# Kernel optimization log

Measured on AMD Instinct MI355X. Metric: run time of the kernel, lower is better.

## Reference

```python
import jax, jax.numpy as jnp
import numpy as np

N = 50000
E = 800000
NODE_IN = 64
EDGE_IN = 8
OUT = 1
SAGE_DIMS = [(64, 64), (64, 64), (64, 32), (32, 32)]
EDGE_DIMS = [(8, 64), (64, 64), (64, 32), (32, 32)]


def setup_inputs():
    key = jax.random.key(0)
    keys = iter(jax.random.split(key, 64))
    d = {}
    d["x"] = jax.random.normal(next(keys), (N, NODE_IN), jnp.float32)
    d["dis"] = jax.random.normal(next(keys), (E, EDGE_IN), jnp.float32)
    d["edge_index"] = jax.random.randint(next(keys), (2, E), 0, N, dtype=jnp.int32)
    for i, (fi, fo) in enumerate(SAGE_DIMS):
        d[f"s{i}_wl"] = jax.random.normal(next(keys), (fi, fo), jnp.float32) / np.sqrt(fi).astype(np.float32)
        d[f"s{i}_bl"] = jnp.zeros((fo,), jnp.float32)
        d[f"s{i}_wr"] = jax.random.normal(next(keys), (fi, fo), jnp.float32) / np.sqrt(fi).astype(np.float32)
    for i, (fi, h) in enumerate(EDGE_DIMS):
        d[f"e{i}_w1"] = jax.random.normal(next(keys), (fi, 2 * h), jnp.float32) / np.sqrt(fi).astype(np.float32)
        d[f"e{i}_b1"] = jnp.zeros((2 * h,), jnp.float32)
        d[f"e{i}_w2"] = jax.random.normal(next(keys), (2 * h, h), jnp.float32) / np.sqrt(2 * h).astype(np.float32)
        d[f"e{i}_b2"] = jnp.zeros((h,), jnp.float32)
    d["fc_w"] = jax.random.normal(next(keys), (64, OUT), jnp.float32) / 8.0
    d["fc_b"] = jnp.zeros((OUT,), jnp.float32)
    return d


def _sage(x, row, col, wl, bl, wr):
    # PyG SAGEConv (aggr='mean'): lin_l(mean_{j->i} x_j) + lin_r(x_i); lin_l has bias.
    msg = x[row]  # [E, F] gather of source features
    s = jax.ops.segment_sum(msg, col, num_segments=N)
    cnt = jax.ops.segment_sum(jnp.ones((row.shape[0], 1), x.dtype), col, num_segments=N)
    mean = s / jnp.maximum(cnt, 1.0)  # isolated nodes -> 0 (matches scatter-mean)
    return mean @ wl + bl + x @ wr


def _edge_conv(dis, col, w1, b1, w2, b2):
    # EdgeOnlyConv: add_self_loops with num_nodes=E and zero edge_attr, so the
    # output has E rows; self-loop message = lin(0) = b1 and each segment t gets
    # mean = (sum_{edges->t} lin(dis) + b1) / (deg_in(t) + 1); then lin_update.
    msg = dis @ w1 + b1  # [E, 2h]
    s = jax.ops.segment_sum(msg, col, num_segments=E)
    deg = jax.ops.segment_sum(jnp.ones((col.shape[0], 1), dis.dtype), col, num_segments=E)
    aggr = (s + b1) / (deg + 1.0)
    return aggr @ w2 + b2


def _forward(x, dis, edge_index, sage_params, edge_params, fc_w, fc_b):
    row, col = edge_index[0], edge_index[1]
    h = x
    for wl, bl, wr in sage_params:
        h = jax.nn.leaky_relu(_sage(h, row, col, wl, bl, wr))
    d = dis
    for w1, b1, w2, b2 in edge_params:
        d = jax.nn.leaky_relu(_edge_conv(d, col, w1, b1, w2, b2))
    # dropout is identity at inference
    feats = jnp.concatenate([h[row] * h[col], d], axis=1)  # [E, hidden]
    return feats @ fc_w + fc_b


def reference(x, dis, edge_index, s0_wl, s0_bl, s0_wr, s1_wl, s1_bl, s1_wr, s2_wl, s2_bl, s2_wr, s3_wl, s3_bl, s3_wr, e0_w1, e0_b1, e0_w2, e0_b2, e1_w1, e1_b1, e1_w2, e1_b2, e2_w1, e2_b1, e2_w2, e2_b2, e3_w1, e3_b1, e3_w2, e3_b2, fc_w, fc_b):
    sage_params = [(s0_wl, s0_bl, s0_wr), (s1_wl, s1_bl, s1_wr), (s2_wl, s2_bl, s2_wr), (s3_wl, s3_bl, s3_wr)]
    edge_params = [(e0_w1, e0_b1, e0_w2, e0_b2), (e1_w1, e1_b1, e1_w2, e1_b2), (e2_w1, e2_b1, e2_w2, e2_b2), (e3_w1, e3_b1, e3_w2, e3_b2)]
    return _forward(x, dis, edge_index, sage_params, edge_params, fc_w, fc_b)
```

## Files before the change

### kernel.cpp

```cpp
#include <hip/hip_runtime.h>

#define LRELU(v) ((v) > 0.0f ? (v) : 0.01f * (v))

__global__ void bucket_count_k(const int* __restrict__ col, int* __restrict__ bcnt, int E) {
    __shared__ int lcnt[512];
    int tid = threadIdx.x;
    for (int i = tid; i < 512; i += 1024) lcnt[i] = 0;
    __syncthreads();
    int base = blockIdx.x * 8192;
    for (int k = 0; k < 8; ++k) {
        int e = base + k * 1024 + tid;
        if (e < E) atomicAdd(&lcnt[col[e] >> 7], 1);
    }
    __syncthreads();
    for (int i = tid; i < 512; i += 1024) {
        int v = lcnt[i];
        if (v) atomicAdd(&bcnt[i], v);
    }
}

__global__ void bucket_scan_k(const int* __restrict__ bcnt, int* __restrict__ bbase,
                              int* __restrict__ bwp, int NBUCK, int E) {
    __shared__ int s[512];
    int tid = threadIdx.x;
    int v = (tid < NBUCK) ? bcnt[tid] : 0;
    s[tid] = v;
    __syncthreads();
    for (int off = 1; off < 512; off <<= 1) {
        int t = (tid >= off) ? s[tid - off] : 0;
        __syncthreads();
        s[tid] += t;
        __syncthreads();
    }
    if (tid < NBUCK) {
        int ex = s[tid] - v;
        bbase[tid] = ex;
        bwp[tid] = ex;
    }
    if (tid == 0) bbase[NBUCK] = E;
}

__global__ void bucket_scatter_k(const int* __restrict__ row, const int* __restrict__ col,
                                 int* __restrict__ bwp, int2* __restrict__ tmp, int E) {
    __shared__ int lcnt[512];
    __shared__ int gbase[512];
    int tid = threadIdx.x;
    for (int i = tid; i < 512; i += 1024) lcnt[i] = 0;
    __syncthreads();
    int base = blockIdx.x * 8192;
    int lpos[8], bk[8];
    for (int k = 0; k < 8; ++k) {
        int e = base + k * 1024 + tid;
        if (e < E) {
            int b = col[e] >> 7;
            bk[k] = b;
            lpos[k] = atomicAdd(&lcnt[b], 1);
        } else
            bk[k] = -1;
    }
    __syncthreads();
    for (int i = tid; i < 512; i += 1024) {
        int v = lcnt[i];
        gbase[i] = v ? atomicAdd(&bwp[i], v) : 0;
    }
    __syncthreads();
    for (int k = 0; k < 8; ++k) {
        int e = base + k * 1024 + tid;
        if (e < E) {
            int c = col[e];
            tmp[gbase[bk[k]] + lpos[k]] = make_int2(row[e], ((c & 127) << 25) | e);
        }
    }
}

__global__ void bucket_csr_k(const int2* __restrict__ tmp, const int* __restrict__ bbase,
                             int* __restrict__ rowptr, int* __restrict__ cnt,
                             int2* __restrict__ pairs, int N, int E) {
    constexpr int CAP = 6144;
    __shared__ int2 buf[CAP];
    __shared__ int lcnt[128];
    __shared__ int sscan[128];
    __shared__ int lwp[128];
    int b = blockIdx.x;
    int tid = threadIdx.x;
    int s = bbase[b], e = bbase[b + 1];
    int sz = e - s;
    if (tid < 128) lcnt[tid] = 0;
    __syncthreads();
    for (int i = tid; i < sz; i += 256) {
        int2 v = tmp[s + i];
        if (i < CAP) buf[i] = v;
        atomicAdd(&lcnt[((unsigned)v.y) >> 25], 1);
    }
    __syncthreads();
    if (tid < 128) sscan[tid] = lcnt[tid];
    __syncthreads();
    for (int off = 1; off < 128; off <<= 1) {
        int t = (tid < 128 && tid >= off) ? sscan[tid - off] : 0;
        __syncthreads();
        if (tid < 128) sscan[tid] += t;
        __syncthreads();
    }
    if (tid < 128) {
        int ex = sscan[tid] - lcnt[tid];
        lwp[tid] = ex;
        int c = b * 128 + tid;
        if (c < N) {
            rowptr[c] = s + ex;
            cnt[c] = lcnt[tid];
            if (c == N - 1) rowptr[N] = E;
        }
    }
    __syncthreads();
    for (int i = tid; i < sz; i += 256) {
        int2 v = (i < CAP) ? buf[i] : tmp[s + i];
        int cl = ((unsigned)v.y) >> 25;
        int p = atomicAdd(&lwp[cl], 1);
        pairs[s + p] = make_int2(v.x, v.y & 0x1FFFFFF);
    }
}

template <int FIN, int FOUT>
__global__ void gemm2_k(const float* __restrict__ h, const float* __restrict__ wl,
                        const float* __restrict__ wr, const float* __restrict__ bl,
                        float* __restrict__ hl, float* __restrict__ hr, int N) {
    constexpr int XT = (2 * FOUT) / 4;
    constexpr int YT = 256 / XT;
    constexpr int NPT = 4;
    constexpr int NPB = YT * NPT;
    __shared__ float sw[FIN * 2 * FOUT];
    int lin = threadIdx.y * XT + threadIdx.x;
    for (int idx = lin; idx < FIN * FOUT; idx += 256) {
        int f = idx / FOUT, o = idx % FOUT;
        sw[f * 2 * FOUT + o] = wl[idx];
        sw[f * 2 * FOUT + FOUT + o] = wr[idx];
    }
    __syncthreads();
    int og = threadIdx.x * 4;
    int base = blockIdx.x * NPB + threadIdx.y * NPT;
    int ix[NPT] = {min(base + 0, N - 1), min(base + 1, N - 1), min(base + 2, N - 1),
                   min(base + 3, N - 1)};
    float4 s[NPT] = {{0.f, 0.f, 0.f, 0.f}, {0.f, 0.f, 0.f, 0.f}, {0.f, 0.f, 0.f, 0.f},
                     {0.f, 0.f, 0.f, 0.f}};
#pragma unroll 2
    for (int f = 0; f < FIN; f += 4) {
        float4 w0 = *(const float4*)&sw[(f + 0) * 2 * FOUT + og];
        float4 w1 = *(const float4*)&sw[(f + 1) * 2 * FOUT + og];
        float4 w2 = *(const float4*)&sw[(f + 2) * 2 * FOUT + og];
        float4 w3 = *(const float4*)&sw[(f + 3) * 2 * FOUT + og];
#pragma unroll
        for (int k = 0; k < NPT; ++k) {
            float4 v = *(const float4*)(h + (size_t)ix[k] * FIN + f);
            s[k].x += v.x * w0.x + v.y * w1.x + v.z * w2.x + v.w * w3.x;
            s[k].y += v.x * w0.y + v.y * w1.y + v.z * w2.y + v.w * w3.y;
            s[k].z += v.x * w0.z + v.y * w1.z + v.z * w2.z + v.w * w3.z;
            s[k].w += v.x * w0.w + v.y * w1.w + v.z * w2.w + v.w * w3.w;
        }
    }
    bool isR = og >= FOUT;
    int oo = isR ? og - FOUT : og;
    float4 bias = {0.f, 0.f, 0.f, 0.f};
    if (isR) bias = *(const float4*)&bl[oo];
    float* dst = isR ? hr : hl;
#pragma unroll
    for (int k = 0; k < NPT; ++k) {
        int i = base + k;
        if (i < N) {
            float4 r = {s[k].x + bias.x, s[k].y + bias.y, s[k].z + bias.z, s[k].w + bias.w};
            *(float4*)(dst + (size_t)i * FOUT + oo) = r;
        }
    }
}

__global__ void aggr_fused64_k(const float* __restrict__ hl, const float* __restrict__ hr,
                               const int* __restrict__ rowptr, const int2* __restrict__ pairs,
                               float* __restrict__ out, int N) {
    int wave = (blockIdx.x * blockDim.x + threadIdx.x) >> 6;
    int lane = threadIdx.x & 63;
    if (wave >= N) return;
    int u = lane >> 4, f4 = lane & 15;
    int s = rowptr[wave], e = rowptr[wave + 1];
    float4 a = {0.f, 0.f, 0.f, 0.f};
    for (int p = s + u; p < e; p += 4) {
        const float4* hp = (const float4*)(hl + (size_t)pairs[p].x * 64);
        float4 v = hp[f4];
        a.x += v.x; a.y += v.y; a.z += v.z; a.w += v.w;
    }
    a.x += __shfl_down(a.x, 32); a.y += __shfl_down(a.y, 32);
    a.z += __shfl_down(a.z, 32); a.w += __shfl_down(a.w, 32);
    a.x += __shfl_down(a.x, 16); a.y += __shfl_down(a.y, 16);
    a.z += __shfl_down(a.z, 16); a.w += __shfl_down(a.w, 16);
    if (lane < 16) {
        float inv = 1.0f / fmaxf((float)(e - s), 1.0f);
        float4 r = ((const float4*)(hr + (size_t)wave * 64))[f4];
        float4 o;
        o.x = LRELU(a.x * inv + r.x);
        o.y = LRELU(a.y * inv + r.y);
        o.z = LRELU(a.z * inv + r.z);
        o.w = LRELU(a.w * inv + r.w);
        ((float4*)(out + (size_t)wave * 64))[f4] = o;
    }
}

__global__ void aggr_fused32_k(const float* __restrict__ hl, const float* __restrict__ hr,
                               const int* __restrict__ rowptr, const int2* __restrict__ pairs,
                               float* __restrict__ out, int N) {
    int wave = (blockIdx.x * blockDim.x + threadIdx.x) >> 6;
    int lane = threadIdx.x & 63;
    if (wave >= N) return;
    int u = lane >> 3, f4 = lane & 7;
    int s = rowptr[wave], e = rowptr[wave + 1];
    float4 a = {0.f, 0.f, 0.f, 0.f};
    for (int p = s + u; p < e; p += 8) {
        const float4* hp = (const float4*)(hl + (size_t)pairs[p].x * 32);
        float4 v = hp[f4];
        a.x += v.x; a.y += v.y; a.z += v.z; a.w += v.w;
    }
    a.x += __shfl_down(a.x, 32); a.y += __shfl_down(a.y, 32);
    a.z += __shfl_down(a.z, 32); a.w += __shfl_down(a.w, 32);
    a.x += __shfl_down(a.x, 16); a.y += __shfl_down(a.y, 16);
    a.z += __shfl_down(a.z, 16); a.w += __shfl_down(a.w, 16);
    a.x += __shfl_down(a.x, 8); a.y += __shfl_down(a.y, 8);
    a.z += __shfl_down(a.z, 8); a.w += __shfl_down(a.w, 8);
    if (lane < 8) {
        float inv = 1.0f / fmaxf((float)(e - s), 1.0f);
        float4 r = ((const float4*)(hr + (size_t)wave * 32))[f4];
        float4 o;
        o.x = LRELU(a.x * inv + r.x);
        o.y = LRELU(a.y * inv + r.y);
        o.z = LRELU(a.z * inv + r.z);
        o.w = LRELU(a.w * inv + r.w);
        ((float4*)(out + (size_t)wave * 32))[f4] = o;
    }
}

__global__ void edge_aggr8_k(const float* __restrict__ dis, const int* __restrict__ rowptr,
                             const int2* __restrict__ pairs, float* __restrict__ sd, int N) {
    int wave = (blockIdx.x * blockDim.x + threadIdx.x) >> 6;
    int lane = threadIdx.x & 63;
    if (wave >= N) return;
    int u = lane >> 1, f4 = lane & 1;
    int s = rowptr[wave], e = rowptr[wave + 1];
    float4 a = {0.f, 0.f, 0.f, 0.f};
    for (int p = s + u; p < e; p += 32) {
        const float4* dp = (const float4*)(dis + (size_t)pairs[p].y * 8);
        float4 v = dp[f4];
        a.x += v.x; a.y += v.y; a.z += v.z; a.w += v.w;
    }
    for (int off = 32; off >= 2; off >>= 1) {
        a.x += __shfl_down(a.x, off); a.y += __shfl_down(a.y, off);
        a.z += __shfl_down(a.z, off); a.w += __shfl_down(a.w, off);
    }
    if (lane < 2) ((float4*)(sd + (size_t)wave * 8))[f4] = a;
}

template <int H2, int HOUT>
__device__ __forceinline__ void w12_body(const float* __restrict__ w1,
                                         const float* __restrict__ w2, float* __restrict__ out,
                                         int i, int o) {
    float s = 0.0f;
#pragma unroll
    for (int k = 0; k < H2; ++k) s += w1[i * H2 + k] * w2[k * HOUT + o];
    out[i * HOUT + o] = s;
}

__global__ void gemm_w12_all_k(const float* __restrict__ w1_0, const float* __restrict__ w2_0,
                               float* __restrict__ o0, const float* __restrict__ w1_1,
                               const float* __restrict__ w2_1, float* __restrict__ o1,
                               const float* __restrict__ w1_2, const float* __restrict__ w2_2,
                               float* __restrict__ o2, const float* __restrict__ w1_3,
                               const float* __restrict__ w2_3, float* __restrict__ o3) {
    int b = blockIdx.x;
    int o = threadIdx.x;
    if (b < 8) {
        w12_body<128, 64>(w1_0, w2_0, o0, b, o);
    } else if (b < 72) {
        w12_body<128, 64>(w1_1, w2_1, o1, b - 8, o);
    } else if (b < 136) {
        if (o < 32) w12_body<64, 32>(w1_2, w2_2, o2, b - 72, o);
    } else {
        if (o < 32) w12_body<64, 32>(w1_3, w2_3, o3, b - 136, o);
    }
}

template <int FIN, int FOUT>
__global__ void edge_compute_scatter_k(const float* __restrict__ sd, const int* __restrict__ cnt,
                                       const float* __restrict__ w12, const float* __restrict__ mw2,
                                       const float* __restrict__ b1w2, const float* __restrict__ b2,
                                       const float* __restrict__ cnext,
                                       const int* __restrict__ col, float* __restrict__ sdnext,
                                       int N) {
    constexpr int ROWS = 256 / FOUT;
    constexpr int NPT = 4;
    constexpr int NPB = ROWS * NPT;
    __shared__ float sw[FIN * FOUT];
    int lin = threadIdx.y * FOUT + threadIdx.x;
    for (int idx = lin; idx < FIN * FOUT; idx += 256) sw[idx] = w12[idx];
    __syncthreads();
    int o = threadIdx.x;
    int base = blockIdx.x * NPB + threadIdx.y * NPT;
    int ix[NPT] = {min(base + 0, N - 1), min(base + 1, N - 1), min(base + 2, N - 1),
                   min(base + 3, N - 1)};
    float s[NPT] = {0.f, 0.f, 0.f, 0.f};
#pragma unroll 2
    for (int f = 0; f < FIN; f += 4) {
        float w0 = sw[(f + 0) * FOUT + o], w1 = sw[(f + 1) * FOUT + o];
        float w2 = sw[(f + 2) * FOUT + o], w3 = sw[(f + 3) * FOUT + o];
#pragma unroll
        for (int k = 0; k < NPT; ++k) {
            float4 v = *(const float4*)(sd + (size_t)ix[k] * FIN + f);
            s[k] += v.x * w0 + v.y * w1 + v.z * w2 + v.w * w3;
        }
    }
    float mo = mw2[o], bo = b1w2[o], b2o = b2[o], co = cnext[o];
#pragma unroll
    for (int k = 0; k < NPT; ++k) {
        int i = base + k;
        if (i < N) {
            float deg = (float)cnt[i];
            float inv = 1.0f / (deg + 1.0f);
            float val = LRELU((s[k] + deg * mo + bo) * inv + b2o);
            atomicAdd(&sdnext[(size_t)col[i] * FOUT + o], val - co);
        }
    }
}

template <int FIN, int FOUT>
__global__ void edge_compute2_k(const float* __restrict__ sd, const int* __restrict__ cnt,
                                const float* __restrict__ w12, const float* __restrict__ mw2,
                                const float* __restrict__ b1w2, const float* __restrict__ b2,
                                float* __restrict__ out, int N) {
    constexpr int ROWS = 256 / FOUT;
    constexpr int NPT = 4;
    constexpr int NPB = ROWS * NPT;
    __shared__ float sw[FIN * FOUT];
    int lin = threadIdx.y * FOUT + threadIdx.x;
    for (int idx = lin; idx < FIN * FOUT; idx += 256) sw[idx] = w12[idx];
    __syncthreads();
    int o = threadIdx.x;
    int base = blockIdx.x * NPB + threadIdx.y * NPT;
    int ix[NPT] = {min(base + 0, N - 1), min(base + 1, N - 1), min(base + 2, N - 1),
                   min(base + 3, N - 1)};
    float s[NPT] = {0.f, 0.f, 0.f, 0.f};
#pragma unroll 2
    for (int f = 0; f < FIN; f += 4) {
        float w0 = sw[(f + 0) * FOUT + o], w1 = sw[(f + 1) * FOUT + o];
        float w2 = sw[(f + 2) * FOUT + o], w3 = sw[(f + 3) * FOUT + o];
#pragma unroll
        for (int k = 0; k < NPT; ++k) {
            float4 v = *(const float4*)(sd + (size_t)ix[k] * FIN + f);
            s[k] += v.x * w0 + v.y * w1 + v.z * w2 + v.w * w3;
        }
    }
    float mo = mw2[o], bo = b1w2[o], b2o = b2[o];
#pragma unroll
    for (int k = 0; k < NPT; ++k) {
        int i = base + k;
        if (i < N) {
            float deg = (float)cnt[i];
            float inv = 1.0f / (deg + 1.0f);
            out[(size_t)i * FOUT + o] = LRELU((s[k] + deg * mo + bo) * inv + b2o);
        }
    }
}

__global__ void consts_k(const float* __restrict__ e0_b1, const float* __restrict__ e0_w2,
                         const float* __restrict__ e0_b2, const float* __restrict__ e1_b1,
                         const float* __restrict__ e1_w2, const float* __restrict__ e1_b2,
                         const float* __restrict__ e2_b1, const float* __restrict__ e2_w2,
                         const float* __restrict__ e2_b2, const float* __restrict__ e3_b1,
                         const float* __restrict__ e3_w2, const float* __restrict__ e3_b2,
                         const float* __restrict__ w12_1, const float* __restrict__ w12_2,
                         const float* __restrict__ w12_3, float* __restrict__ cbuf) {
    __shared__ float c1[64], c2[64], c3[32];
    int tid = threadIdx.x;
    if (tid < 64) {
        float s = 0.0f;
#pragma unroll
        for (int k = 0; k < 128; ++k) s += e0_b1[k] * e0_w2[k * 64 + tid];
        cbuf[192 + tid] = s;
        c1[tid] = LRELU(s + e0_b2[tid]);
        cbuf[tid] = c1[tid];
    }
    if (tid < 64) {
        float s = 0.0f;
#pragma unroll
        for (int k = 0; k < 128; ++k) s += e1_b1[k] * e1_w2[k * 64 + tid];
        cbuf[256 + tid] = s;
        c2[tid] = LRELU(s + e1_b2[tid]);
        cbuf[64 + tid] = c2[tid];
    }
    if (tid < 32) {
        float s = 0.0f;
#pragma unroll
        for (int k = 0; k < 64; ++k) s += e2_b1[k] * e2_w2[k * 32 + tid];
        cbuf[384 + tid] = s;
        c3[tid] = LRELU(s + e2_b2[tid]);
        cbuf[128 + tid] = c3[tid];
    }
    if (tid < 32) {
        float s = 0.0f;
#pragma unroll
        for (int k = 0; k < 64; ++k) s += e3_b1[k] * e3_w2[k * 32 + tid];
        cbuf[448 + tid] = s;
        cbuf[160 + tid] = LRELU(s + e3_b2[tid]);
    }
    __syncthreads();
    if (tid < 64) {
        float s = cbuf[256 + tid];
#pragma unroll
        for (int f = 0; f < 64; ++f) s += c1[f] * w12_1[f * 64 + tid];
        cbuf[320 + tid] = s;
    }
    if (tid < 32) {
        float s = cbuf[384 + tid];
#pragma unroll
        for (int f = 0; f < 64; ++f) s += c2[f] * w12_2[f * 32 + tid];
        cbuf[416 + tid] = s;
    }
    if (tid < 32) {
        float s = cbuf[448 + tid];
#pragma unroll
        for (int f = 0; f < 32; ++f) s += c3[f] * w12_3[f * 32 + tid];
        cbuf[480 + tid] = s;
    }
}

__global__ void tobf16_k(const float* __restrict__ src, unsigned short* __restrict__ dst, int n) {
    int base = (blockIdx.x * 256 + threadIdx.x) * 4;
    if (base >= n) return;
    float4 v = *(const float4*)(src + base);
    union { float f; unsigned u; } c;
    unsigned short o[4];
    c.f = v.x; o[0] = (unsigned short)((c.u + 0x7fffu + ((c.u >> 16) & 1)) >> 16);
    c.f = v.y; o[1] = (unsigned short)((c.u + 0x7fffu + ((c.u >> 16) & 1)) >> 16);
    c.f = v.z; o[2] = (unsigned short)((c.u + 0x7fffu + ((c.u >> 16) & 1)) >> 16);
    c.f = v.w; o[3] = (unsigned short)((c.u + 0x7fffu + ((c.u >> 16) & 1)) >> 16);
    *(ushort4*)(dst + base) = make_ushort4(o[0], o[1], o[2], o[3]);
}

__device__ __forceinline__ float b2f_lo(unsigned u) {
    union { unsigned i; float f; } v;
    v.i = u << 16;
    return v.f;
}
__device__ __forceinline__ float b2f_hi(unsigned u) {
    union { unsigned i; float f; } v;
    v.i = u & 0xffff0000u;
    return v.f;
}
__device__ __forceinline__ float bdot8(uint4 a, uint4 b, const float* __restrict__ w) {
    return b2f_lo(a.x) * b2f_lo(b.x) * w[0] + b2f_hi(a.x) * b2f_hi(b.x) * w[1] +
           b2f_lo(a.y) * b2f_lo(b.y) * w[2] + b2f_hi(a.y) * b2f_hi(b.y) * w[3] +
           b2f_lo(a.z) * b2f_lo(b.z) * w[4] + b2f_hi(a.z) * b2f_hi(b.z) * w[5] +
           b2f_lo(a.w) * b2f_lo(b.w) * w[6] + b2f_hi(a.w) * b2f_hi(b.w) * w[7];
}

__global__ void final_k(const unsigned short* __restrict__ h3b, const float* __restrict__ dv3,
                        const float* __restrict__ c4, const int* __restrict__ row,
                        const int* __restrict__ col, const float* __restrict__ fcw,
                        const float* __restrict__ fcb, float* __restrict__ out, int E, int N) {
    __shared__ float sw[64];
    __shared__ float sc4[32];
    __shared__ float cdot_s;
    int tid = threadIdx.x;
    if (tid < 64) sw[tid] = fcw[tid];
    if (tid < 32) sc4[tid] = c4[tid];
    __syncthreads();
    if (tid == 0) {
        float cd = 0.0f;
#pragma unroll
        for (int k = 0; k < 32; ++k) cd += sc4[k] * sw[32 + k];
        cdot_s = cd;
    }
    __syncthreads();
    float fb = fcb[0];
    float cdot = cdot_s;
    int e0 = blockIdx.x * 512 + tid;
    int e1 = e0 + 256;
    bool v0 = e0 < E, v1 = e1 < E;
    int r0 = 0, c0 = 0, r1 = 0, c1 = 0;
    if (v0) { r0 = row[e0]; c0 = col[e0]; }
    if (v1) { r1 = row[e1]; c1 = col[e1]; }
    uint4 a00, a01, b00, b01, a10, a11, b10, b11;
    if (v0) {
        const uint4* pr = (const uint4*)(h3b + (size_t)r0 * 32);
        const uint4* pc = (const uint4*)(h3b + (size_t)c0 * 32);
        a00 = pr[0]; a01 = pr[1]; b00 = pc[0]; b01 = pc[1];
    }
    if (v1) {
        const uint4* pr = (const uint4*)(h3b + (size_t)r1 * 32);
        const uint4* pc = (const uint4*)(h3b + (size_t)c1 * 32);
        a10 = pr[0]; a11 = pr[1]; b10 = pc[0]; b11 = pc[1];
    }
    if (v0) {
        float s = fb + bdot8(a00, b00, sw) + bdot8(a01, b01, sw + 8) ;
        const uint4* pr = (const uint4*)(h3b + (size_t)r0 * 32);
        const uint4* pc = (const uint4*)(h3b + (size_t)c0 * 32);
        uint4 a2 = pr[2], a3 = pr[3], b2 = pc[2], b3 = pc[3];
        s += bdot8(a2, b2, sw + 16) + bdot8(a3, b3, sw + 24);
        if (e0 < N) {
            const float4* dp = (const float4*)(dv3 + (size_t)e0 * 32);
#pragma unroll
            for (int q = 0; q < 8; ++q) {
                float4 d = dp[q];
                s += d.x * sw[32 + q * 4 + 0] + d.y * sw[32 + q * 4 + 1] +
                     d.z * sw[32 + q * 4 + 2] + d.w * sw[32 + q * 4 + 3];
            }
        } else {
            s += cdot;
        }
        out[e0] = s;
    }
    if (v1) {
        float s = fb + bdot8(a10, b10, sw) + bdot8(a11, b11, sw + 8);
        const uint4* pr = (const uint4*)(h3b + (size_t)r1 * 32);
        const uint4* pc = (const uint4*)(h3b + (size_t)c1 * 32);
        uint4 a2 = pr[2], a3 = pr[3], b2 = pc[2], b3 = pc[3];
        s += bdot8(a2, b2, sw + 16) + bdot8(a3, b3, sw + 24);
        if (e1 < N) {
            const float4* dp = (const float4*)(dv3 + (size_t)e1 * 32);
#pragma unroll
            for (int q = 0; q < 8; ++q) {
                float4 d = dp[q];
                s += d.x * sw[32 + q * 4 + 0] + d.y * sw[32 + q * 4 + 1] +
                     d.z * sw[32 + q * 4 + 2] + d.w * sw[32 + q * 4 + 3];
            }
        } else {
            s += cdot;
        }
        out[e1] = s;
    }
}

extern "C" void kernel_launch(void* const* d_in, const int* in_sizes, int n_in, void* d_out,
                              int out_size, void* d_ws, size_t ws_size, hipStream_t stream) {
    const float* x = (const float*)d_in[0];
    const float* dis = (const float*)d_in[1];
    const int* ei = (const int*)d_in[2];
    const float* s_wl[4] = {(const float*)d_in[3], (const float*)d_in[6], (const float*)d_in[9],
                            (const float*)d_in[12]};
    const float* s_bl[4] = {(const float*)d_in[4], (const float*)d_in[7], (const float*)d_in[10],
                            (const float*)d_in[13]};
    const float* s_wr[4] = {(const float*)d_in[5], (const float*)d_in[8], (const float*)d_in[11],
                            (const float*)d_in[14]};
    const float* e_w1[4] = {(const float*)d_in[15], (const float*)d_in[19], (const float*)d_in[23],
                            (const float*)d_in[27]};
    const float* e_b1[4] = {(const float*)d_in[16], (const float*)d_in[20], (const float*)d_in[24],
                            (const float*)d_in[28]};
    const float* e_w2[4] = {(const float*)d_in[17], (const float*)d_in[21], (const float*)d_in[25],
                            (const float*)d_in[29]};
    const float* e_b2[4] = {(const float*)d_in[18], (const float*)d_in[22], (const float*)d_in[26],
                            (const float*)d_in[30]};
    const float* fcw = (const float*)d_in[31];
    const float* fcb = (const float*)d_in[32];

    const int N = in_sizes[0] / 64;
    const int E = in_sizes[1] / 8;
    const int* row = ei;
    const int* col = ei + E;
    const int NBUCK = (N + 127) / 128;
    const int EB = (E + 8191) / 8192;

    auto au = [](size_t v) { return (v + 255) & ~(size_t)255; };
    char* p = (char*)d_ws;
    int* cnt = (int*)p;       p += au((size_t)N * 4);
    int* rowptr = (int*)p;    p += au((size_t)(N + 1) * 4);
    int* bcnt = (int*)p;      p += au(512 * 4);
    int* bbase = (int*)p;     p += au(513 * 4);
    int* bwp = (int*)p;       p += au(512 * 4);
    float* w12_0 = (float*)p; p += au(512 * 4);
    float* w12_1 = (float*)p; p += au(4096 * 4);
    float* w12_2 = (float*)p; p += au(2048 * 4);
    float* w12_3 = (float*)p; p += au(1024 * 4);
    float* cbuf = (float*)p;  p += au(512 * 4);
    int2* pairs = (int2*)p;   p += au((size_t)E * 8);
    float* acc = (float*)p;   p += au((size_t)N * 64 * 4);
    float* hA = (float*)p;    p += au((size_t)N * 64 * 4);
    float* hB = (float*)p;    p += au((size_t)N * 64 * 4);
    float* dvA = (float*)p;   p += au((size_t)N * 64 * 4);
    float* dvB = (float*)p;   p += au((size_t)N * 64 * 4);

    int2* tmp = (int2*)dvA;
    unsigned short* h3b = (unsigned short*)hA;

    hipMemsetAsync(bcnt, 0, 512 * 4, stream);
    bucket_count_k<<<EB, 1024, 0, stream>>>(col, bcnt, E);
    bucket_scan_k<<<1, 512, 0, stream>>>(bcnt, bbase, bwp, NBUCK, E);
    bucket_scatter_k<<<EB, 1024, 0, stream>>>(row, col, bwp, tmp, E);
    bucket_csr_k<<<NBUCK, 256, 0, stream>>>(tmp, bbase, rowptr, cnt, pairs, N, E);

    gemm_w12_all_k<<<168, 64, 0, stream>>>(e_w1[0], e_w2[0], w12_0, e_w1[1], e_w2[1], w12_1,
                                           e_w1[2], e_w2[2], w12_2, e_w1[3], e_w2[3], w12_3);
    consts_k<<<1, 128, 0, stream>>>(e_b1[0], e_w2[0], e_b2[0], e_b1[1], e_w2[1], e_b2[1], e_b1[2],
                                    e_w2[2], e_b2[2], e_b1[3], e_w2[3], e_b2[3], w12_1, w12_2,
                                    w12_3, cbuf);

    const int WPB = 4;

    gemm2_k<64, 64><<<(N + 31) / 32, dim3(32, 8), 0, stream>>>(x, s_wl[0], s_wr[0], s_bl[0], acc,
                                                               dvB, N);
    aggr_fused64_k<<<(N + WPB - 1) / WPB, 256, 0, stream>>>(acc, dvB, rowptr, pairs, hA, N);
    gemm2_k<64, 64><<<(N + 31) / 32, dim3(32, 8), 0, stream>>>(hA, s_wl[1], s_wr[1], s_bl[1], acc,
                                                               dvB, N);
    aggr_fused64_k<<<(N + WPB - 1) / WPB, 256, 0, stream>>>(acc, dvB, rowptr, pairs, hB, N);
    gemm2_k<64, 32><<<(N + 63) / 64, dim3(16, 16), 0, stream>>>(hB, s_wl[2], s_wr[2], s_bl[2], acc,
                                                                dvB, N);
    aggr_fused32_k<<<(N + WPB - 1) / WPB, 256, 0, stream>>>(acc, dvB, rowptr, pairs, hA, N);
    gemm2_k<32, 32><<<(N + 63) / 64, dim3(16, 16), 0, stream>>>(hA, s_wl[3], s_wr[3], s_bl[3], acc,
                                                                dvB, N);
    aggr_fused32_k<<<(N + WPB - 1) / WPB, 256, 0, stream>>>(acc, dvB, rowptr, pairs, hB, N);

    tobf16_k<<<(N * 32 / 4 + 255) / 256, 256, 0, stream>>>(hB, h3b, N * 32);

    edge_aggr8_k<<<(N + WPB - 1) / WPB, 256, 0, stream>>>(dis, rowptr, pairs, acc, N);
    hipMemsetAsync(dvA, 0, (size_t)N * 64 * 4, stream);
    edge_compute_scatter_k<8, 64><<<(N + 15) / 16, dim3(64, 4), 0, stream>>>(
        acc, cnt, w12_0, cbuf + 192, cbuf + 192, e_b2[0], cbuf + 0, col, dvA, N);
    hipMemsetAsync(acc, 0, (size_t)N * 64 * 4, stream);
    edge_compute_scatter_k<64, 64><<<(N + 15) / 16, dim3(64, 4), 0, stream>>>(
        dvA, cnt, w12_1, cbuf + 320, cbuf + 256, e_b2[1], cbuf + 64, col, acc, N);
    hipMemsetAsync(dvA, 0, (size_t)N * 32 * 4, stream);
    edge_compute_scatter_k<64, 32><<<(N + 31) / 32, dim3(32, 8), 0, stream>>>(
        acc, cnt, w12_2, cbuf + 416, cbuf + 384, e_b2[2], cbuf + 128, col, dvA, N);
    edge_compute2_k<32, 32><<<(N + 31) / 32, dim3(32, 8), 0, stream>>>(
        dvA, cnt, w12_3, cbuf + 480, cbuf + 448, e_b2[3], dvB, N);

    final_k<<<(E + 511) / 512, 256, 0, stream>>>(h3b, dvB, cbuf + 160, row, col, fcw, fcb,
                                                 (float*)d_out, E, N);
}
```

Before: 505.6 us.

## Store gathered SAGE features in bf16 and fuse final bf16 conversion

The first two SAGE layers now write the left-projected features (the ones gathered per edge) as bf16, and the aggregation kernel reads and widens them, halving gather bytes over 800k edges. The last aggregation writes its output directly in bf16, which removes the separate tobf16 conversion kernel and one full pass over the features. The cost is reduced precision in the aggregated neighbour sums for layers 0 and 1.

```diff
diff --git a/kernel.cpp b/kernel.cpp
--- a/kernel.cpp
+++ b/kernel.cpp
@@ -1,6 +1,22 @@
 #include <hip/hip_runtime.h>
 
 #define LRELU(v) ((v) > 0.0f ? (v) : 0.01f * (v))
+
+__device__ __forceinline__ unsigned short f2bf(float f) {
+    union { float f; unsigned u; } c;
+    c.f = f;
+    return (unsigned short)((c.u + 0x7fffu + ((c.u >> 16) & 1)) >> 16);
+}
+__device__ __forceinline__ float bf_lo(unsigned u) {
+    union { unsigned i; float f; } v;
+    v.i = u << 16;
+    return v.f;
+}
+__device__ __forceinline__ float bf_hi(unsigned u) {
+    union { unsigned i; float f; } v;
+    v.i = u & 0xffff0000u;
+    return v.f;
+}
 
 __global__ void bucket_count_k(const int* __restrict__ col, int* __restrict__ bcnt, int E) {
     __shared__ int lcnt[512];
@@ -120,10 +136,10 @@
     }
 }
 
-template <int FIN, int FOUT>
+template <int FIN, int FOUT, bool BFL>
 __global__ void gemm2_k(const float* __restrict__ h, const float* __restrict__ wl,
                         const float* __restrict__ wr, const float* __restrict__ bl,
-                        float* __restrict__ hl, float* __restrict__ hr, int N) {
+                        void* __restrict__ hl, float* __restrict__ hr, int N) {
     constexpr int XT = (2 * FOUT) / 4;
     constexpr int YT = 256 / XT;
     constexpr int NPT = 4;
@@ -159,22 +175,36 @@
     }
     bool isR = og >= FOUT;
     int oo = isR ? og - FOUT : og;
-    float4 bias = {0.f, 0.f, 0.f, 0.f};
-    if (isR) bias = *(const float4*)&bl[oo];
-    float* dst = isR ? hr : hl;
-#pragma unroll
-    for (int k = 0; k < NPT; ++k) {
-        int i = base + k;
-        if (i < N) {
-            float4 r = {s[k].x + bias.x, s[k].y + bias.y, s[k].z + bias.z, s[k].w + bias.w};
-            *(float4*)(dst + (size_t)i * FOUT + oo) = r;
-        }
-    }
-}
-
-__global__ void aggr_fused64_k(const float* __restrict__ hl, const float* __restrict__ hr,
-                               const int* __restrict__ rowptr, const int2* __restrict__ pairs,
-                               float* __restrict__ out, int N) {
+    if (isR) {
+        float4 bias = *(const float4*)&bl[oo];
+#pragma unroll
+        for (int k = 0; k < NPT; ++k) {
+            int i = base + k;
+            if (i < N) {
+                float4 r = {s[k].x + bias.x, s[k].y + bias.y, s[k].z + bias.z, s[k].w + bias.w};
+                *(float4*)(hr + (size_t)i * FOUT + oo) = r;
+            }
+        }
+    } else {
+#pragma unroll
+        for (int k = 0; k < NPT; ++k) {
+            int i = base + k;
+            if (i < N) {
+                if (BFL) {
+                    unsigned short* d = (unsigned short*)hl + (size_t)i * FOUT + oo;
+                    *(ushort4*)d =
+                        make_ushort4(f2bf(s[k].x), f2bf(s[k].y), f2bf(s[k].z), f2bf(s[k].w));
+                } else {
+                    *(float4*)((float*)hl + (size_t)i * FOUT + oo) = s[k];
+                }
+            }
+        }
+    }
+}
+
+__global__ void aggr_fused64_bf_k(const unsigned short* __restrict__ hlb,
+                                  const float* __restrict__ hr, const int* __restrict__ rowptr,
+                                  const int2* __restrict__ pairs, float* __restrict__ out, int N) {
     int wave = (blockIdx.x * blockDim.x + threadIdx.x) >> 6;
     int lane = threadIdx.x & 63;
     if (wave >= N) return;
@@ -182,9 +212,8 @@
     int s = rowptr[wave], e = rowptr[wave + 1];
     float4 a = {0.f, 0.f, 0.f, 0.f};
     for (int p = s + u; p < e; p += 4) {
-        const float4* hp = (const float4*)(hl + (size_t)pairs[p].x * 64);
-        float4 v = hp[f4];
-        a.x += v.x; a.y += v.y; a.z += v.z; a.w += v.w;
+        uint2 v = ((const uint2*)(hlb + (size_t)pairs[p].x * 64))[f4];
+        a.x += bf_lo(v.x); a.y += bf_hi(v.x); a.z += bf_lo(v.y); a.w += bf_hi(v.y);
     }
     a.x += __shfl_down(a.x, 32); a.y += __shfl_down(a.y, 32);
     a.z += __shfl_down(a.z, 32); a.w += __shfl_down(a.w, 32);
@@ -202,9 +231,10 @@
     }
 }
 
+template <bool OUTBF>
 __global__ void aggr_fused32_k(const float* __restrict__ hl, const float* __restrict__ hr,
                                const int* __restrict__ rowptr, const int2* __restrict__ pairs,
-                               float* __restrict__ out, int N) {
+                               void* __restrict__ out, int N) {
     int wave = (blockIdx.x * blockDim.x + threadIdx.x) >> 6;
     int lane = threadIdx.x & 63;
     if (wave >= N) return;
@@ -230,7 +260,12 @@
         o.y = LRELU(a.y * inv + r.y);
         o.z = LRELU(a.z * inv + r.z);
         o.w = LRELU(a.w * inv + r.w);
-        ((float4*)(out + (size_t)wave * 32))[f4] = o;
+        if (OUTBF) {
+            unsigned short* d = (unsigned short*)out + (size_t)wave * 32 + f4 * 4;
+            *(ushort4*)d = make_ushort4(f2bf(o.x), f2bf(o.y), f2bf(o.z), f2bf(o.w));
+        } else {
+            ((float4*)((float*)out + (size_t)wave * 32))[f4] = o;
+        }
     }
 }
 
@@ -426,34 +461,11 @@
     }
 }
 
-__global__ void tobf16_k(const float* __restrict__ src, unsigned short* __restrict__ dst, int n) {
-    int base = (blockIdx.x * 256 + threadIdx.x) * 4;
-    if (base >= n) return;
-    float4 v = *(const float4*)(src + base);
-    union { float f; unsigned u; } c;
-    unsigned short o[4];
-    c.f = v.x; o[0] = (unsigned short)((c.u + 0x7fffu + ((c.u >> 16) & 1)) >> 16);
-    c.f = v.y; o[1] = (unsigned short)((c.u + 0x7fffu + ((c.u >> 16) & 1)) >> 16);
-    c.f = v.z; o[2] = (unsigned short)((c.u + 0x7fffu + ((c.u >> 16) & 1)) >> 16);
-    c.f = v.w; o[3] = (unsigned short)((c.u + 0x7fffu + ((c.u >> 16) & 1)) >> 16);
-    *(ushort4*)(dst + base) = make_ushort4(o[0], o[1], o[2], o[3]);
-}
-
-__device__ __forceinline__ float b2f_lo(unsigned u) {
-    union { unsigned i; float f; } v;
-    v.i = u << 16;
-    return v.f;
-}
-__device__ __forceinline__ float b2f_hi(unsigned u) {
-    union { unsigned i; float f; } v;
-    v.i = u & 0xffff0000u;
-    return v.f;
-}
 __device__ __forceinline__ float bdot8(uint4 a, uint4 b, const float* __restrict__ w) {
-    return b2f_lo(a.x) * b2f_lo(b.x) * w[0] + b2f_hi(a.x) * b2f_hi(b.x) * w[1] +
-           b2f_lo(a.y) * b2f_lo(b.y) * w[2] + b2f_hi(a.y) * b2f_hi(b.y) * w[3] +
-           b2f_lo(a.z) * b2f_lo(b.z) * w[4] + b2f_hi(a.z) * b2f_hi(b.z) * w[5] +
-           b2f_lo(a.w) * b2f_lo(b.w) * w[6] + b2f_hi(a.w) * b2f_hi(b.w) * w[7];
+    return bf_lo(a.x) * bf_lo(b.x) * w[0] + bf_hi(a.x) * bf_hi(b.x) * w[1] +
+           bf_lo(a.y) * bf_lo(b.y) * w[2] + bf_hi(a.y) * bf_hi(b.y) * w[3] +
+           bf_lo(a.z) * bf_lo(b.z) * w[4] + bf_hi(a.z) * bf_hi(b.z) * w[5] +
+           bf_lo(a.w) * bf_lo(b.w) * w[6] + bf_hi(a.w) * bf_hi(b.w) * w[7];
 }
 
 __global__ void final_k(const unsigned short* __restrict__ h3b, const float* __restrict__ dv3,
@@ -494,11 +506,11 @@
         a10 = pr[0]; a11 = pr[1]; b10 = pc[0]; b11 = pc[1];
     }
     if (v0) {
-        float s = fb + bdot8(a00, b00, sw) + bdot8(a01, b01, sw + 8) ;
-        const uint4* pr = (const uint4*)(h3b + (size_t)r0 * 32);
-        const uint4* pc = (const uint4*)(h3b + (size_t)c0 * 32);
-        uint4 a2 = pr[2], a3 = pr[3], b2 = pc[2], b3 = pc[3];
-        s += bdot8(a2, b2, sw + 16) + bdot8(a3, b3, sw + 24);
+        float s = fb + bdot8(a00, b00, sw) + bdot8(a01, b01, sw + 8) +
+                  bdot8(((const uint4*)(h3b + (size_t)r0 * 32))[2],
+                        ((const uint4*)(h3b + (size_t)c0 * 32))[2], sw + 16) +
+                  bdot8(((const uint4*)(h3b + (size_t)r0 * 32))[3],
+                        ((const uint4*)(h3b + (size_t)c0 * 32))[3], sw + 24);
         if (e0 < N) {
             const float4* dp = (const float4*)(dv3 + (size_t)e0 * 32);
 #pragma unroll
@@ -513,11 +525,11 @@
         out[e0] = s;
     }
     if (v1) {
-        float s = fb + bdot8(a10, b10, sw) + bdot8(a11, b11, sw + 8);
-        const uint4* pr = (const uint4*)(h3b + (size_t)r1 * 32);
-        const uint4* pc = (const uint4*)(h3b + (size_t)c1 * 32);
-        uint4 a2 = pr[2], a3 = pr[3], b2 = pc[2], b3 = pc[3];
-        s += bdot8(a2, b2, sw + 16) + bdot8(a3, b3, sw + 24);
+        float s = fb + bdot8(a10, b10, sw) + bdot8(a11, b11, sw + 8) +
+                  bdot8(((const uint4*)(h3b + (size_t)r1 * 32))[2],
+                        ((const uint4*)(h3b + (size_t)c1 * 32))[2], sw + 16) +
+                  bdot8(((const uint4*)(h3b + (size_t)r1 * 32))[3],
+                        ((const uint4*)(h3b + (size_t)c1 * 32))[3], sw + 24);
         if (e1 < N) {
             const float4* dp = (const float4*)(dv3 + (size_t)e1 * 32);
 #pragma unroll
@@ -582,6 +594,7 @@
     float* dvB = (float*)p;   p += au((size_t)N * 64 * 4);
 
     int2* tmp = (int2*)dvA;
+    unsigned short* hlb = (unsigned short*)acc;
     unsigned short* h3b = (unsigned short*)hA;
 
     hipMemsetAsync(bcnt, 0, 512 * 4, stream);
@@ -598,20 +611,18 @@
 
     const int WPB = 4;
 
-    gemm2_k<64, 64><<<(N + 31) / 32, dim3(32, 8), 0, stream>>>(x, s_wl[0], s_wr[0], s_bl[0], acc,
-                                                               dvB, N);
-    aggr_fused64_k<<<(N + WPB - 1) / WPB, 256, 0, stream>>>(acc, dvB, rowptr, pairs, hA, N);
-    gemm2_k<64, 64><<<(N + 31) / 32, dim3(32, 8), 0, stream>>>(hA, s_wl[1], s_wr[1], s_bl[1], acc,
-                                                               dvB, N);
-    aggr_fused64_k<<<(N + WPB - 1) / WPB, 256, 0, stream>>>(acc, dvB, rowptr, pairs, hB, N);
-    gemm2_k<64, 32><<<(N + 63) / 64, dim3(16, 16), 0, stream>>>(hB, s_wl[2], s_wr[2], s_bl[2], acc,
-                                                                dvB, N);
-    aggr_fused32_k<<<(N + WPB - 1) / WPB, 256, 0, stream>>>(acc, dvB, rowptr, pairs, hA, N);
-    gemm2_k<32, 32><<<(N + 63) / 64, dim3(16, 16), 0, stream>>>(hA, s_wl[3], s_wr[3], s_bl[3], acc,
-                                                                dvB, N);
-    aggr_fused32_k<<<(N + WPB - 1) / WPB, 256, 0, stream>>>(acc, dvB, rowptr, pairs, hB, N);
-
-    tobf16_k<<<(N * 32 / 4 + 255) / 256, 256, 0, stream>>>(hB, h3b, N * 32);
+    gemm2_k<64, 64, true><<<(N + 31) / 32, dim3(32, 8), 0, stream>>>(x, s_wl[0], s_wr[0], s_bl[0],
+                                                                     hlb, dvB, N);
+    aggr_fused64_bf_k<<<(N + WPB - 1) / WPB, 256, 0, stream>>>(hlb, dvB, rowptr, pairs, hA, N);
+    gemm2_k<64, 64, true><<<(N + 31) / 32, dim3(32, 8), 0, stream>>>(hA, s_wl[1], s_wr[1], s_bl[1],
+                                                                     hlb, dvB, N);
+    aggr_fused64_bf_k<<<(N + WPB - 1) / WPB, 256, 0, stream>>>(hlb, dvB, rowptr, pairs, hB, N);
+    gemm2_k<64, 32, false><<<(N + 63) / 64, dim3(16, 16), 0, stream>>>(hB, s_wl[2], s_wr[2],
+                                                                       s_bl[2], acc, dvB, N);
+    aggr_fused32_k<false><<<(N + WPB - 1) / WPB, 256, 0, stream>>>(acc, dvB, rowptr, pairs, hA, N);
+    gemm2_k<32, 32, false><<<(N + 63) / 64, dim3(16, 16), 0, stream>>>(hA, s_wl[3], s_wr[3],
+                                                                       s_bl[3], acc, dvB, N);
+    aggr_fused32_k<true><<<(N + WPB - 1) / WPB, 256, 0, stream>>>(acc, dvB, rowptr, pairs, h3b, N);
 
     edge_aggr8_k<<<(N + WPB - 1) / WPB, 256, 0, stream>>>(dis, rowptr, pairs, acc, N);
     hipMemsetAsync(dvA, 0, (size_t)N * 64 * 4, stream);
```

Result: no change. 498.4 us (-1.4%).
